# Kernel tuning notes

Hardware: AMD Instinct MI355X
Metric: run time of the kernel (lower is better)

Reference implementation:

```python
import jax, jax.numpy as jnp
import numpy as np

H = 32        # query heads
KVH = 8       # kv heads
HD = 64       # head_dim
N_REP = H // KVH
THETA = 10000.0


def _rope_cos_sin(seq_len, dim):
    # freqs_cis[t, i] = exp(1j * t * theta^{-2i/dim}) -> return cos, sin [S, dim//2]
    inv_freq = 1.0 / (THETA ** (jnp.arange(0, dim, 2, dtype=jnp.float32) / dim))
    t = jnp.arange(seq_len, dtype=jnp.float32)
    freqs = jnp.outer(t, inv_freq)  # [S, dim//2]
    return jnp.cos(freqs), jnp.sin(freqs)


def _apply_rope(x, cos, sin):
    # x: [B, S, h, HD]; pairs are interleaved (even=real, odd=imag)
    xr = x[..., 0::2]
    xi = x[..., 1::2]
    c = cos[None, :, None, :]
    s = sin[None, :, None, :]
    out_r = xr * c - xi * s
    out_i = xr * s + xi * c
    return jnp.stack([out_r, out_i], axis=-1).reshape(x.shape)


def setup_inputs() -> dict:
    key = jax.random.key(0)
    ks = jax.random.split(key, 5)
    D = 2048
    B, S = 1, 2048
    scale = 0.02
    return {
        "hidden_states": jax.random.normal(ks[0], (B, S, D), jnp.float32),
        "Wq": jax.random.normal(ks[1], (D, H * HD), jnp.float32) * scale,
        "Wk": jax.random.normal(ks[2], (D, KVH * HD), jnp.float32) * scale,
        "Wv": jax.random.normal(ks[3], (D, KVH * HD), jnp.float32) * scale,
        "Wo": jax.random.normal(ks[4], (H * HD, D), jnp.float32) * scale,
    }


def reference(hidden_states, Wq, Wk, Wv, Wo):
    B, S, D = hidden_states.shape
    xq = (hidden_states @ Wq).reshape(B, S, H, HD)
    xk = (hidden_states @ Wk).reshape(B, S, KVH, HD)
    xv = (hidden_states @ Wv).reshape(B, S, KVH, HD)

    cos, sin = _rope_cos_sin(S, HD)
    xq = _apply_rope(xq, cos, sin)
    xk = _apply_rope(xk, cos, sin)

    # GQA: expand kv heads (kv head g -> query heads g*N_REP .. g*N_REP+N_REP-1)
    keys = jnp.repeat(xk, N_REP, axis=2)    # [B, S, H, HD]
    values = jnp.repeat(xv, N_REP, axis=2)

    q = xq.transpose(0, 2, 1, 3)      # [B, H, S, HD]
    k = keys.transpose(0, 2, 1, 3)
    v = values.transpose(0, 2, 1, 3)

    scores = jnp.einsum('bhqd,bhkd->bhqk', q, k) / jnp.sqrt(jnp.float32(HD))
    causal = jnp.tril(jnp.ones((S, S), dtype=bool))
    scores = jnp.where(causal[None, None], scores, jnp.float32(-jnp.inf))
    probs = jax.nn.softmax(scores.astype(jnp.float32), axis=-1).astype(q.dtype)

    out = jnp.einsum('bhqk,bhkd->bhqd', probs, v)   # [B, H, S, HD]
    out = out.transpose(0, 2, 1, 3).reshape(B, S, H * HD)
    return out @ Wo
```

## Files before the change

kernel.cpp:

```cpp
#include <hip/hip_runtime.h>


#define S_LEN  2048
#define NH     32
#define NKV    8

typedef __attribute__((ext_vector_type(8))) __bf16 bf16x8;
typedef __attribute__((ext_vector_type(4))) __bf16 bf16x4;
typedef __attribute__((ext_vector_type(4))) float  f32x4;

#define SCALE_LOG2 0.18033688011112042f
#define L2_10K_32  0.41524101186098665f

__device__ __forceinline__ void glds16(const __bf16* g, __bf16* l) {
  __builtin_amdgcn_global_load_lds(
      (const __attribute__((address_space(1))) unsigned int*)g,
      (__attribute__((address_space(3))) unsigned int*)l, 16, 0, 0);
}

__global__ void k_f32_to_bf16(const float* __restrict__ src,
                              __bf16* __restrict__ dst, int n) {
  int i = (blockIdx.x * blockDim.x + threadIdx.x) * 4;
  if (i >= n) return;
  float4 v = *(const float4*)(src + i);
  bf16x4 o;
  o[0] = (__bf16)v.x; o[1] = (__bf16)v.y; o[2] = (__bf16)v.z; o[3] = (__bf16)v.w;
  *(bf16x4*)(dst + i) = o;
}

__global__ void k_wtrans(const float* __restrict__ W, int ldW,
                         __bf16* __restrict__ Wt) {
  __shared__ float t[32][33];
  int n0 = blockIdx.x * 32, k0 = blockIdx.y * 32;
  int tx = threadIdx.x, ty = threadIdx.y;
#pragma unroll
  for (int j = 0; j < 4; j++)
    t[ty + j * 8][tx] = W[(size_t)(k0 + ty + j * 8) * ldW + n0 + tx];
  __syncthreads();
#pragma unroll
  for (int j = 0; j < 4; j++)
    Wt[(size_t)(n0 + ty + j * 8) * 2048 + k0 + tx] = (__bf16)t[tx][ty + j * 8];
}

__global__ void k_vtrans_b(const __bf16* __restrict__ V, __bf16* __restrict__ Vt) {
  __shared__ __bf16 t[32][33];
  int c0 = blockIdx.x * 32, s0 = blockIdx.y * 32;
  int tx = threadIdx.x, ty = threadIdx.y;
#pragma unroll
  for (int j = 0; j < 4; j++)
    t[ty + j * 8][tx] = V[(size_t)(s0 + ty + j * 8) * 512 + c0 + tx];
  __syncthreads();
#pragma unroll
  for (int j = 0; j < 4; j++)
    Vt[(size_t)(c0 + ty + j * 8) * 2048 + s0 + tx] = t[tx][ty + j * 8];
}

__global__ void k_add2(const float* __restrict__ a, const float* __restrict__ b,
                       float* __restrict__ out, int n) {
  int i = (blockIdx.x * blockDim.x + threadIdx.x) * 4;
  if (i >= n) return;
  float4 x = *(const float4*)(a + i);
  float4 y = *(const float4*)(b + i);
  x.x += y.x; x.y += y.y; x.z += y.z; x.w += y.w;
  *(float4*)(out + i) = x;
}

__global__ __launch_bounds__(256) void k_gemm_qkv(
    const __bf16* __restrict__ A, const __bf16* __restrict__ Bt,
    __bf16* __restrict__ Qb, __bf16* __restrict__ Kb, __bf16* __restrict__ Vb) {
  const int K = 2048, N = 3072;
  __shared__ __bf16 As[128][32];
  __shared__ __bf16 Bs[128][32];
  const int tid = threadIdx.x;
  const int m0 = blockIdx.x * 128, n0 = blockIdx.y * 128;
  const int w = tid >> 6, lane = tid & 63, quad = lane >> 4, lid = lane & 15;
  const int wm = (w & 1) * 64, wn = (w >> 1) * 64;
  const int r0 = tid >> 2;
  const int cg = (((tid & 3) ^ ((tid >> 3) & 3)) * 8);
  const __bf16* Ag = A + (size_t)(m0 + r0) * K + cg;
  const __bf16* Bg = Bt + (size_t)(n0 + r0) * K + cg;
  __bf16* Asl = &As[0][0] + tid * 8;
  __bf16* Bsl = &Bs[0][0] + tid * 8;
  const int csw = ((quad ^ ((lid >> 1) & 3)) * 8);
  f32x4 acc[4][4] = {};
  for (int k0 = 0; k0 < K; k0 += 32) {
    __syncthreads();
    glds16(Ag + k0, Asl);
    glds16(Ag + (size_t)64 * K + k0, Asl + 2048);
    glds16(Bg + k0, Bsl);
    glds16(Bg + (size_t)64 * K + k0, Bsl + 2048);
    __syncthreads();
    bf16x8 a[4], b[4];
#pragma unroll
    for (int mt = 0; mt < 4; mt++)
      a[mt] = *(const bf16x8*)(&As[wm + mt * 16 + lid][csw]);
#pragma unroll
    for (int nt = 0; nt < 4; nt++)
      b[nt] = *(const bf16x8*)(&Bs[wn + nt * 16 + lid][csw]);
#pragma unroll
    for (int mt = 0; mt < 4; mt++)
#pragma unroll
      for (int nt = 0; nt < 4; nt++)
        acc[mt][nt] = __builtin_amdgcn_mfma_f32_16x16x32_bf16(
            a[mt], b[nt], acc[mt][nt], 0, 0, 0);
  }
  if (n0 >= 2560) {
#pragma unroll
    for (int mt = 0; mt < 4; mt++)
#pragma unroll
      for (int nt = 0; nt < 4; nt++)
#pragma unroll
        for (int i = 0; i < 4; i++) {
          int mm = m0 + wm + mt * 16 + quad * 4 + i;
          int nn = n0 + wn + nt * 16 + lid - 2560;
          Vb[(size_t)mm * 512 + nn] = (__bf16)acc[mt][nt][i];
        }
  } else {
    const bool isQ = (n0 < 2048);
    const float scale = isQ ? SCALE_LOG2 : 1.0f;
    __bf16* dst = isQ ? Qb : Kb;
    const int ldd = isQ ? 2048 : 512;
    const int noff = isQ ? 0 : 2048;
    const bool odd = lid & 1;
#pragma unroll
    for (int nt = 0; nt < 4; nt++) {
      int nn = n0 + wn + nt * 16 + lid;
      int fi = (nn & 63) >> 1;
      float inv = __builtin_amdgcn_exp2f(-(float)fi * L2_10K_32);
#pragma unroll
      for (int mt = 0; mt < 4; mt++)
#pragma unroll
        for (int i = 0; i < 4; i++) {
          int mm = m0 + wm + mt * 16 + quad * 4 + i;
          float ang = (float)mm * inv;
          float sn, cs;
          __sincosf(ang, &sn, &cs);
          float v = acc[mt][nt][i];
          float p = __shfl_xor(v, 1);
          float o = v * cs + (odd ? p : -p) * sn;
          dst[(size_t)mm * ldd + nn - noff] = (__bf16)(o * scale);
        }
    }
  }
}

__global__ __launch_bounds__(256) void k_gemm(
    const __bf16* __restrict__ A, const __bf16* __restrict__ Bt,
    float* __restrict__ C, int M, int N, int K, int klen) {
  __shared__ __bf16 As[128][32];
  __shared__ __bf16 Bs[128][32];
  const int tid = threadIdx.x;
  const int m0 = blockIdx.x * 128, n0 = blockIdx.y * 128;
  const size_t koff = (size_t)blockIdx.z * klen;
  C += (size_t)blockIdx.z * M * N;
  const int w = tid >> 6, lane = tid & 63, quad = lane >> 4, lid = lane & 15;
  const int wm = (w & 1) * 64, wn = (w >> 1) * 64;
  const int r0 = tid >> 2;
  const int cg = (((tid & 3) ^ ((tid >> 3) & 3)) * 8);
  const __bf16* Ag = A + (size_t)(m0 + r0) * K + koff + cg;
  const __bf16* Bg = Bt + (size_t)(n0 + r0) * K + koff + cg;
  __bf16* Asl = &As[0][0] + tid * 8;
  __bf16* Bsl = &Bs[0][0] + tid * 8;
  const int csw = ((quad ^ ((lid >> 1) & 3)) * 8);
  f32x4 acc[4][4] = {};
  for (int k0 = 0; k0 < klen; k0 += 32) {
    __syncthreads();
    glds16(Ag + k0, Asl);
    glds16(Ag + (size_t)64 * K + k0, Asl + 2048);
    glds16(Bg + k0, Bsl);
    glds16(Bg + (size_t)64 * K + k0, Bsl + 2048);
    __syncthreads();
    bf16x8 a[4], b[4];
#pragma unroll
    for (int mt = 0; mt < 4; mt++)
      a[mt] = *(const bf16x8*)(&As[wm + mt * 16 + lid][csw]);
#pragma unroll
    for (int nt = 0; nt < 4; nt++)
      b[nt] = *(const bf16x8*)(&Bs[wn + nt * 16 + lid][csw]);
#pragma unroll
    for (int mt = 0; mt < 4; mt++)
#pragma unroll
      for (int nt = 0; nt < 4; nt++)
        acc[mt][nt] = __builtin_amdgcn_mfma_f32_16x16x32_bf16(
            a[mt], b[nt], acc[mt][nt], 0, 0, 0);
  }
#pragma unroll
  for (int mt = 0; mt < 4; mt++)
#pragma unroll
    for (int nt = 0; nt < 4; nt++)
#pragma unroll
      for (int i = 0; i < 4; i++) {
        int mm = m0 + wm + mt * 16 + quad * 4 + i;
        int nn = n0 + wn + nt * 16 + lid;
        C[(size_t)mm * N + nn] = acc[mt][nt][i];
      }
}

__global__ __launch_bounds__(256) void k_attn(
    const __bf16* __restrict__ Q, const __bf16* __restrict__ Kc,
    const __bf16* __restrict__ Vt, __bf16* __restrict__ Oc) {
  __shared__ __bf16 Qs[64][64];
  __shared__ __bf16 Ks[2][64][64];
  __shared__ __bf16 Vs[2][64][64];
  __shared__ __bf16 Ps[4][16][72];
  const int h = blockIdx.x;
  const int qt = (gridDim.y - 1) - blockIdx.y;
  const int q0 = qt * 64;
  const int kvh = h >> 2;
  const int tid = threadIdx.x;
  const int w = tid >> 6, lane = tid & 63, quad = lane >> 4, lid = lane & 15;
  const int r0 = tid >> 3;
  const int cg0 = (((tid & 7) ^ (r0 & 7)) * 8);

  const __bf16* Qg = Q + (size_t)(q0 + r0) * 2048 + h * 64 + cg0;
  const __bf16* Kg = Kc + kvh * 64 + cg0;
  const __bf16* Vg = Vt + ((size_t)kvh * 64 + r0) * 2048 + cg0;

  glds16(Qg, &Qs[0][0] + tid * 8);
  glds16(Qg + (size_t)32 * 2048, &Qs[0][0] + (tid + 256) * 8);
  glds16(Kg + (size_t)r0 * 512, &Ks[0][0][0] + tid * 8);
  glds16(Kg + (size_t)(r0 + 32) * 512, &Ks[0][0][0] + (tid + 256) * 8);
  glds16(Vg, &Vs[0][0][0] + tid * 8);
  glds16(Vg + (size_t)32 * 2048, &Vs[0][0][0] + (tid + 256) * 8);
  __syncthreads();

  const int clq = (quad ^ (lid & 7)) * 8;
  bf16x8 aq0 = *(const bf16x8*)(&Qs[w * 16 + lid][clq]);
  bf16x8 aq1 = *(const bf16x8*)(&Qs[w * 16 + lid][clq ^ 32]);
  bf16x8 bone;
#pragma unroll
  for (int j = 0; j < 8; j++) bone[j] = (lid == 0) ? (__bf16)1.0f : (__bf16)0.0f;

  f32x4 Oacc[4] = {};
  f32x4 Lacc = {};
  float mi[4];
#pragma unroll
  for (int i = 0; i < 4; i++) mi[i] = -1e30f;

  for (int kt = 0; kt <= qt; kt++) {
    const int cb = kt & 1;
    if (kt < qt) {
      const int nb = cb ^ 1;
      const size_t kv1 = (size_t)(kt + 1) * 64;
      glds16(Kg + (kv1 + r0) * 512, &Ks[nb][0][0] + tid * 8);
      glds16(Kg + (kv1 + r0 + 32) * 512, &Ks[nb][0][0] + (tid + 256) * 8);
      glds16(Vg + kv1, &Vs[nb][0][0] + tid * 8);
      glds16(Vg + (size_t)32 * 2048 + kv1, &Vs[nb][0][0] + (tid + 256) * 8);
    }

    f32x4 Sc[4] = {};
#pragma unroll
    for (int nt = 0; nt < 4; nt++) {
      bf16x8 b0 = *(const bf16x8*)(&Ks[cb][nt * 16 + lid][clq]);
      bf16x8 b1 = *(const bf16x8*)(&Ks[cb][nt * 16 + lid][clq ^ 32]);
      Sc[nt] = __builtin_amdgcn_mfma_f32_16x16x32_bf16(aq0, b0, Sc[nt], 0, 0, 0);
      Sc[nt] = __builtin_amdgcn_mfma_f32_16x16x32_bf16(aq1, b1, Sc[nt], 0, 0, 0);
    }
    if (kt == qt) {
#pragma unroll
      for (int nt = 0; nt < 4; nt++)
#pragma unroll
        for (int i = 0; i < 4; i++) {
          int kvcol = nt * 16 + lid, qrow = w * 16 + quad * 4 + i;
          if (kvcol > qrow) Sc[nt][i] = -1e30f;
        }
    }

    float alpha[4];
#pragma unroll
    for (int i = 0; i < 4; i++) {
      float m = fmaxf(fmaxf(Sc[0][i], Sc[1][i]), fmaxf(Sc[2][i], Sc[3][i]));
#pragma unroll
      for (int off = 1; off < 16; off <<= 1) m = fmaxf(m, __shfl_xor(m, off));
      float mnew = fmaxf(mi[i], m);
      alpha[i] = __builtin_amdgcn_exp2f(mi[i] - mnew);
      mi[i] = mnew;
    }
#pragma unroll
    for (int nt = 0; nt < 4; nt++)
#pragma unroll
      for (int i = 0; i < 4; i++) {
        float p = __builtin_amdgcn_exp2f(Sc[nt][i] - mi[i]);
        Ps[w][quad * 4 + i][nt * 16 + lid] = (__bf16)p;
      }
#pragma unroll
    for (int nt = 0; nt < 4; nt++)
#pragma unroll
      for (int i = 0; i < 4; i++) Oacc[nt][i] *= alpha[i];
#pragma unroll
    for (int i = 0; i < 4; i++) Lacc[i] *= alpha[i];

#pragma unroll
    for (int kc = 0; kc < 2; kc++) {
      bf16x8 ap = *(const bf16x8*)(&Ps[w][lid][kc * 32 + quad * 8]);
      Lacc = __builtin_amdgcn_mfma_f32_16x16x32_bf16(ap, bone, Lacc, 0, 0, 0);
#pragma unroll
      for (int nt = 0; nt < 4; nt++) {
        bf16x8 bv = *(const bf16x8*)(
            &Vs[cb][nt * 16 + lid][(((kc * 4 + quad) ^ (lid & 7)) * 8)]);
        Oacc[nt] = __builtin_amdgcn_mfma_f32_16x16x32_bf16(ap, bv, Oacc[nt], 0, 0, 0);
      }
    }
    __syncthreads();
  }

#pragma unroll
  for (int nt = 0; nt < 4; nt++)
#pragma unroll
    for (int i = 0; i < 4; i++) {
      float li = __shfl(Lacc[i], lane & 48);
      int qrow = q0 + w * 16 + quad * 4 + i;
      int hd = nt * 16 + lid;
      Oc[(size_t)qrow * 2048 + h * 64 + hd] = (__bf16)(Oacc[nt][i] / li);
    }
}

extern "C" void kernel_launch(void* const* d_in, const int* in_sizes, int n_in,
                              void* d_out, int out_size, void* d_ws, size_t ws_size,
                              hipStream_t stream) {
  const float* hx = (const float*)d_in[0];
  const float* Wq = (const float*)d_in[1];
  const float* Wk = (const float*)d_in[2];
  const float* Wv = (const float*)d_in[3];
  const float* Wo = (const float*)d_in[4];
  float* out = (float*)d_out;

  char* ws = (char*)d_ws;
  size_t off = 0;
  auto alloc = [&](size_t bytes) -> void* {
    void* p = ws + off;
    off += (bytes + 255) & ~(size_t)255;
    return p;
  };
  __bf16* Xb    = (__bf16*)alloc((size_t)2048 * 2048 * 2);
  __bf16* Wqkvt = (__bf16*)alloc((size_t)3072 * 2048 * 2);
  __bf16* Wot   = (__bf16*)alloc((size_t)2048 * 2048 * 2);
  __bf16* Qb    = (__bf16*)alloc((size_t)2048 * 2048 * 2);
  __bf16* Kb    = (__bf16*)alloc((size_t)2048 * 512 * 2);
  __bf16* Vb    = (__bf16*)alloc((size_t)2048 * 512 * 2);
  __bf16* Vtg   = (__bf16*)alloc((size_t)512 * 2048 * 2);
  __bf16* AOb   = (__bf16*)alloc((size_t)2048 * 2048 * 2);
  float*  Cf0   = (float*)alloc((size_t)2048 * 2048 * 4);
  float*  Cf1   = (float*)alloc((size_t)2048 * 2048 * 4);

  k_f32_to_bf16<<<4096, 256, 0, stream>>>(hx, Xb, 2048 * 2048);
  k_wtrans<<<dim3(64, 64), dim3(32, 8), 0, stream>>>(Wq, 2048, Wqkvt);
  k_wtrans<<<dim3(16, 64), dim3(32, 8), 0, stream>>>(Wk, 512, Wqkvt + (size_t)2048 * 2048);
  k_wtrans<<<dim3(16, 64), dim3(32, 8), 0, stream>>>(Wv, 512, Wqkvt + (size_t)2560 * 2048);
  k_wtrans<<<dim3(64, 64), dim3(32, 8), 0, stream>>>(Wo, 2048, Wot);
  k_gemm_qkv<<<dim3(16, 24), 256, 0, stream>>>(Xb, Wqkvt, Qb, Kb, Vb);
  k_vtrans_b<<<dim3(16, 64), dim3(32, 8), 0, stream>>>(Vb, Vtg);
  k_attn<<<dim3(NH, S_LEN / 64), 256, 0, stream>>>(Qb, Kb, Vtg, AOb);
  k_gemm<<<dim3(16, 16, 2), 256, 0, stream>>>(AOb, Wot, Cf0, 2048, 2048, 2048, 1024);
  k_add2<<<4096, 256, 0, stream>>>(Cf0, Cf1, out, 2048 * 2048);
}
```

Baseline: 245.2 us.

## Fuse prep kernels, retile GEMMs, drop split-K, widen attention query tile

Folds the input cast and the four weight transposes into a single prep launch. Shrinks the M tile of both GEMMs to 64 so more blocks run, and drops split-K plus the add kernel so the output GEMM writes the result directly. Attention now processes 128 query rows per block with two m-tiles per wave, uses DPP for the row max and pair swaps, and aliases Q with the P buffer in LDS. Together these cut launches and intermediate traffic and raise data reuse, but the larger attention blocks reduce grid size and may lower occupancy.

```diff
diff --git a/kernel.cpp b/kernel.cpp
--- a/kernel.cpp
+++ b/kernel.cpp
@@ -1,12 +1,10 @@
 #include <hip/hip_runtime.h>
 
 
-#define S_LEN  2048
-#define NH     32
-#define NKV    8
+#define NH  32
+#define NKV 8
 
 typedef __attribute__((ext_vector_type(8))) __bf16 bf16x8;
-typedef __attribute__((ext_vector_type(4))) __bf16 bf16x4;
 typedef __attribute__((ext_vector_type(4))) float  f32x4;
 
 #define SCALE_LOG2 0.18033688011112042f
@@ -18,28 +16,58 @@
       (__attribute__((address_space(3))) unsigned int*)l, 16, 0, 0);
 }
 
-__global__ void k_f32_to_bf16(const float* __restrict__ src,
-                              __bf16* __restrict__ dst, int n) {
-  int i = (blockIdx.x * blockDim.x + threadIdx.x) * 4;
-  if (i >= n) return;
-  float4 v = *(const float4*)(src + i);
-  bf16x4 o;
-  o[0] = (__bf16)v.x; o[1] = (__bf16)v.y; o[2] = (__bf16)v.z; o[3] = (__bf16)v.w;
-  *(bf16x4*)(dst + i) = o;
-}
-
-__global__ void k_wtrans(const float* __restrict__ W, int ldW,
-                         __bf16* __restrict__ Wt) {
+__device__ __forceinline__ float qmax16(float v) {
+  int t;
+  t = __builtin_amdgcn_mov_dpp(__builtin_bit_cast(int, v), 0x128, 0xf, 0xf, true);
+  v = fmaxf(v, __builtin_bit_cast(float, t));
+  t = __builtin_amdgcn_mov_dpp(__builtin_bit_cast(int, v), 0x124, 0xf, 0xf, true);
+  v = fmaxf(v, __builtin_bit_cast(float, t));
+  t = __builtin_amdgcn_mov_dpp(__builtin_bit_cast(int, v), 0x122, 0xf, 0xf, true);
+  v = fmaxf(v, __builtin_bit_cast(float, t));
+  t = __builtin_amdgcn_mov_dpp(__builtin_bit_cast(int, v), 0x121, 0xf, 0xf, true);
+  v = fmaxf(v, __builtin_bit_cast(float, t));
+  return v;
+}
+
+__device__ __forceinline__ float pair_swap(float v) {
+  int t = __builtin_amdgcn_mov_dpp(__builtin_bit_cast(int, v), 0xB1, 0xf, 0xf, true);
+  return __builtin_bit_cast(float, t);
+}
+
+__device__ __forceinline__ unsigned pack_bf16(float lo, float hi) {
+  union { __bf16 b[2]; unsigned u; } r;
+  r.b[0] = (__bf16)lo; r.b[1] = (__bf16)hi;
+  return r.u;
+}
+
+__global__ void k_prep(const float* __restrict__ hx, const float* __restrict__ Wq,
+                       const float* __restrict__ Wk, const float* __restrict__ Wv,
+                       const float* __restrict__ Wo, __bf16* __restrict__ Xb,
+                       __bf16* __restrict__ Wqkvt, __bf16* __restrict__ Wot) {
   __shared__ float t[32][33];
-  int n0 = blockIdx.x * 32, k0 = blockIdx.y * 32;
-  int tx = threadIdx.x, ty = threadIdx.y;
+  const int nt = blockIdx.x, k0 = blockIdx.y * 32;
+  const int tx = threadIdx.x, ty = threadIdx.y;
+  if (nt >= 160) {
+    int c0 = (nt - 160) * 32;
+#pragma unroll
+    for (int j = 0; j < 4; j++) {
+      size_t idx = (size_t)(k0 + ty + j * 8) * 2048 + c0 + tx;
+      Xb[idx] = (__bf16)hx[idx];
+    }
+    return;
+  }
+  const float* W; int ldW, n0; __bf16* dst;
+  if (nt < 64)      { W = Wq; ldW = 2048; dst = Wqkvt;                        n0 = nt * 32; }
+  else if (nt < 80) { W = Wk; ldW = 512;  dst = Wqkvt + (size_t)2048 * 2048;  n0 = (nt - 64) * 32; }
+  else if (nt < 96) { W = Wv; ldW = 512;  dst = Wqkvt + (size_t)2560 * 2048;  n0 = (nt - 80) * 32; }
+  else              { W = Wo; ldW = 2048; dst = Wot;                          n0 = (nt - 96) * 32; }
 #pragma unroll
   for (int j = 0; j < 4; j++)
     t[ty + j * 8][tx] = W[(size_t)(k0 + ty + j * 8) * ldW + n0 + tx];
   __syncthreads();
 #pragma unroll
   for (int j = 0; j < 4; j++)
-    Wt[(size_t)(n0 + ty + j * 8) * 2048 + k0 + tx] = (__bf16)t[tx][ty + j * 8];
+    dst[(size_t)(n0 + ty + j * 8) * 2048 + k0 + tx] = (__bf16)t[tx][ty + j * 8];
 }
 
 __global__ void k_vtrans_b(const __bf16* __restrict__ V, __bf16* __restrict__ Vt) {
@@ -55,26 +83,16 @@
     Vt[(size_t)(c0 + ty + j * 8) * 2048 + s0 + tx] = t[tx][ty + j * 8];
 }
 
-__global__ void k_add2(const float* __restrict__ a, const float* __restrict__ b,
-                       float* __restrict__ out, int n) {
-  int i = (blockIdx.x * blockDim.x + threadIdx.x) * 4;
-  if (i >= n) return;
-  float4 x = *(const float4*)(a + i);
-  float4 y = *(const float4*)(b + i);
-  x.x += y.x; x.y += y.y; x.z += y.z; x.w += y.w;
-  *(float4*)(out + i) = x;
-}
-
 __global__ __launch_bounds__(256) void k_gemm_qkv(
     const __bf16* __restrict__ A, const __bf16* __restrict__ Bt,
     __bf16* __restrict__ Qb, __bf16* __restrict__ Kb, __bf16* __restrict__ Vb) {
-  const int K = 2048, N = 3072;
-  __shared__ __bf16 As[128][32];
+  const int K = 2048;
+  __shared__ __bf16 As[64][32];
   __shared__ __bf16 Bs[128][32];
   const int tid = threadIdx.x;
-  const int m0 = blockIdx.x * 128, n0 = blockIdx.y * 128;
+  const int m0 = blockIdx.x * 64, n0 = blockIdx.y * 128;
   const int w = tid >> 6, lane = tid & 63, quad = lane >> 4, lid = lane & 15;
-  const int wm = (w & 1) * 64, wn = (w >> 1) * 64;
+  const int wm = (w & 1) * 32, wn = (w >> 1) * 64;
   const int r0 = tid >> 2;
   const int cg = (((tid & 3) ^ ((tid >> 3) & 3)) * 8);
   const __bf16* Ag = A + (size_t)(m0 + r0) * K + cg;
@@ -82,23 +100,22 @@
   __bf16* Asl = &As[0][0] + tid * 8;
   __bf16* Bsl = &Bs[0][0] + tid * 8;
   const int csw = ((quad ^ ((lid >> 1) & 3)) * 8);
-  f32x4 acc[4][4] = {};
+  f32x4 acc[2][4] = {};
   for (int k0 = 0; k0 < K; k0 += 32) {
     __syncthreads();
     glds16(Ag + k0, Asl);
-    glds16(Ag + (size_t)64 * K + k0, Asl + 2048);
     glds16(Bg + k0, Bsl);
     glds16(Bg + (size_t)64 * K + k0, Bsl + 2048);
     __syncthreads();
-    bf16x8 a[4], b[4];
-#pragma unroll
-    for (int mt = 0; mt < 4; mt++)
+    bf16x8 a[2], b[4];
+#pragma unroll
+    for (int mt = 0; mt < 2; mt++)
       a[mt] = *(const bf16x8*)(&As[wm + mt * 16 + lid][csw]);
 #pragma unroll
     for (int nt = 0; nt < 4; nt++)
       b[nt] = *(const bf16x8*)(&Bs[wn + nt * 16 + lid][csw]);
 #pragma unroll
-    for (int mt = 0; mt < 4; mt++)
+    for (int mt = 0; mt < 2; mt++)
 #pragma unroll
       for (int nt = 0; nt < 4; nt++)
         acc[mt][nt] = __builtin_amdgcn_mfma_f32_16x16x32_bf16(
@@ -106,7 +123,7 @@
   }
   if (n0 >= 2560) {
 #pragma unroll
-    for (int mt = 0; mt < 4; mt++)
+    for (int mt = 0; mt < 2; mt++)
 #pragma unroll
       for (int nt = 0; nt < 4; nt++)
 #pragma unroll
@@ -128,7 +145,7 @@
       int fi = (nn & 63) >> 1;
       float inv = __builtin_amdgcn_exp2f(-(float)fi * L2_10K_32);
 #pragma unroll
-      for (int mt = 0; mt < 4; mt++)
+      for (int mt = 0; mt < 2; mt++)
 #pragma unroll
         for (int i = 0; i < 4; i++) {
           int mm = m0 + wm + mt * 16 + quad * 4 + i;
@@ -144,48 +161,46 @@
   }
 }
 
-__global__ __launch_bounds__(256) void k_gemm(
+__global__ __launch_bounds__(256) void k_gemm_out(
     const __bf16* __restrict__ A, const __bf16* __restrict__ Bt,
-    float* __restrict__ C, int M, int N, int K, int klen) {
-  __shared__ __bf16 As[128][32];
+    float* __restrict__ C) {
+  const int K = 2048, N = 2048;
+  __shared__ __bf16 As[64][32];
   __shared__ __bf16 Bs[128][32];
   const int tid = threadIdx.x;
-  const int m0 = blockIdx.x * 128, n0 = blockIdx.y * 128;
-  const size_t koff = (size_t)blockIdx.z * klen;
-  C += (size_t)blockIdx.z * M * N;
+  const int m0 = blockIdx.x * 64, n0 = blockIdx.y * 128;
   const int w = tid >> 6, lane = tid & 63, quad = lane >> 4, lid = lane & 15;
-  const int wm = (w & 1) * 64, wn = (w >> 1) * 64;
+  const int wm = (w & 1) * 32, wn = (w >> 1) * 64;
   const int r0 = tid >> 2;
   const int cg = (((tid & 3) ^ ((tid >> 3) & 3)) * 8);
-  const __bf16* Ag = A + (size_t)(m0 + r0) * K + koff + cg;
-  const __bf16* Bg = Bt + (size_t)(n0 + r0) * K + koff + cg;
+  const __bf16* Ag = A + (size_t)(m0 + r0) * K + cg;
+  const __bf16* Bg = Bt + (size_t)(n0 + r0) * K + cg;
   __bf16* Asl = &As[0][0] + tid * 8;
   __bf16* Bsl = &Bs[0][0] + tid * 8;
   const int csw = ((quad ^ ((lid >> 1) & 3)) * 8);
-  f32x4 acc[4][4] = {};
-  for (int k0 = 0; k0 < klen; k0 += 32) {
+  f32x4 acc[2][4] = {};
+  for (int k0 = 0; k0 < K; k0 += 32) {
     __syncthreads();
     glds16(Ag + k0, Asl);
-    glds16(Ag + (size_t)64 * K + k0, Asl + 2048);
     glds16(Bg + k0, Bsl);
     glds16(Bg + (size_t)64 * K + k0, Bsl + 2048);
     __syncthreads();
-    bf16x8 a[4], b[4];
-#pragma unroll
-    for (int mt = 0; mt < 4; mt++)
+    bf16x8 a[2], b[4];
+#pragma unroll
+    for (int mt = 0; mt < 2; mt++)
       a[mt] = *(const bf16x8*)(&As[wm + mt * 16 + lid][csw]);
 #pragma unroll
     for (int nt = 0; nt < 4; nt++)
       b[nt] = *(const bf16x8*)(&Bs[wn + nt * 16 + lid][csw]);
 #pragma unroll
-    for (int mt = 0; mt < 4; mt++)
+    for (int mt = 0; mt < 2; mt++)
 #pragma unroll
       for (int nt = 0; nt < 4; nt++)
         acc[mt][nt] = __builtin_amdgcn_mfma_f32_16x16x32_bf16(
             a[mt], b[nt], acc[mt][nt], 0, 0, 0);
   }
 #pragma unroll
-  for (int mt = 0; mt < 4; mt++)
+  for (int mt = 0; mt < 2; mt++)
 #pragma unroll
     for (int nt = 0; nt < 4; nt++)
 #pragma unroll
@@ -199,13 +214,15 @@
 __global__ __launch_bounds__(256) void k_attn(
     const __bf16* __restrict__ Q, const __bf16* __restrict__ Kc,
     const __bf16* __restrict__ Vt, __bf16* __restrict__ Oc) {
-  __shared__ __bf16 Qs[64][64];
-  __shared__ __bf16 Ks[2][64][64];
-  __shared__ __bf16 Vs[2][64][64];
-  __shared__ __bf16 Ps[4][16][72];
+  __shared__ char smem[51200];
+  __bf16* PsB = (__bf16*)smem;
+  __bf16* QsB = (__bf16*)smem;
+  __bf16* KsB = (__bf16*)(smem + 18432);
+  __bf16* VsB = (__bf16*)(smem + 34816);
   const int h = blockIdx.x;
-  const int qt = (gridDim.y - 1) - blockIdx.y;
-  const int q0 = qt * 64;
+  const int qt = 15 - blockIdx.y;
+  const int q0 = qt * 128;
+  const int nkv = 2 * qt + 2;
   const int kvh = h >> 2;
   const int tid = threadIdx.x;
   const int w = tid >> 6, lane = tid & 63, quad = lane >> 4, lid = lane & 15;
@@ -214,104 +231,158 @@
 
   const __bf16* Qg = Q + (size_t)(q0 + r0) * 2048 + h * 64 + cg0;
   const __bf16* Kg = Kc + kvh * 64 + cg0;
-  const __bf16* Vg = Vt + ((size_t)kvh * 64 + r0) * 2048 + cg0;
-
-  glds16(Qg, &Qs[0][0] + tid * 8);
-  glds16(Qg + (size_t)32 * 2048, &Qs[0][0] + (tid + 256) * 8);
-  glds16(Kg + (size_t)r0 * 512, &Ks[0][0][0] + tid * 8);
-  glds16(Kg + (size_t)(r0 + 32) * 512, &Ks[0][0][0] + (tid + 256) * 8);
-  glds16(Vg, &Vs[0][0][0] + tid * 8);
-  glds16(Vg + (size_t)32 * 2048, &Vs[0][0][0] + (tid + 256) * 8);
+  const __bf16* Vg = Vt + ((size_t)(kvh * 64 + r0)) * 2048 + cg0;
+
+  glds16(Qg,                     QsB + tid * 8);
+  glds16(Qg + (size_t)32 * 2048, QsB + (tid + 256) * 8);
+  glds16(Qg + (size_t)64 * 2048, QsB + (tid + 512) * 8);
+  glds16(Qg + (size_t)96 * 2048, QsB + (tid + 768) * 8);
+  glds16(Kg + (size_t)r0 * 512,        KsB + tid * 8);
+  glds16(Kg + (size_t)(r0 + 32) * 512, KsB + (tid + 256) * 8);
+  glds16(Vg,                     VsB + tid * 8);
+  glds16(Vg + (size_t)32 * 2048, VsB + (tid + 256) * 8);
   __syncthreads();
 
-  const int clq = (quad ^ (lid & 7)) * 8;
-  bf16x8 aq0 = *(const bf16x8*)(&Qs[w * 16 + lid][clq]);
-  bf16x8 aq1 = *(const bf16x8*)(&Qs[w * 16 + lid][clq ^ 32]);
+  bf16x8 aq[2][2];
+#pragma unroll
+  for (int mt = 0; mt < 2; mt++) {
+    int row = w * 32 + mt * 16 + lid;
+    int cl = (quad ^ (row & 7)) * 8;
+    aq[mt][0] = *(const bf16x8*)(QsB + row * 64 + cl);
+    aq[mt][1] = *(const bf16x8*)(QsB + row * 64 + (cl ^ 32));
+  }
+  __syncthreads();
+
   bf16x8 bone;
 #pragma unroll
   for (int j = 0; j < 8; j++) bone[j] = (lid == 0) ? (__bf16)1.0f : (__bf16)0.0f;
 
-  f32x4 Oacc[4] = {};
-  f32x4 Lacc = {};
-  float mi[4];
-#pragma unroll
-  for (int i = 0; i < 4; i++) mi[i] = -1e30f;
-
-  for (int kt = 0; kt <= qt; kt++) {
+  f32x4 Oacc[2][4] = {};
+  f32x4 Lacc[2] = {};
+  float mi[2][4];
+#pragma unroll
+  for (int mt = 0; mt < 2; mt++)
+#pragma unroll
+    for (int i = 0; i < 4; i++) mi[mt][i] = -1e30f;
+
+  for (int kt = 0; kt < nkv; kt++) {
     const int cb = kt & 1;
-    if (kt < qt) {
+    if (kt + 1 < nkv) {
       const int nb = cb ^ 1;
       const size_t kv1 = (size_t)(kt + 1) * 64;
-      glds16(Kg + (kv1 + r0) * 512, &Ks[nb][0][0] + tid * 8);
-      glds16(Kg + (kv1 + r0 + 32) * 512, &Ks[nb][0][0] + (tid + 256) * 8);
-      glds16(Vg + kv1, &Vs[nb][0][0] + tid * 8);
-      glds16(Vg + (size_t)32 * 2048 + kv1, &Vs[nb][0][0] + (tid + 256) * 8);
-    }
-
-    f32x4 Sc[4] = {};
+      glds16(Kg + (kv1 + r0) * 512,        KsB + nb * 4096 + tid * 8);
+      glds16(Kg + (kv1 + r0 + 32) * 512,   KsB + nb * 4096 + (tid + 256) * 8);
+      glds16(Vg + kv1,                     VsB + nb * 4096 + tid * 8);
+      glds16(Vg + (size_t)32 * 2048 + kv1, VsB + nb * 4096 + (tid + 256) * 8);
+    }
+
+    f32x4 Sc[2][4] = {};
 #pragma unroll
     for (int nt = 0; nt < 4; nt++) {
-      bf16x8 b0 = *(const bf16x8*)(&Ks[cb][nt * 16 + lid][clq]);
-      bf16x8 b1 = *(const bf16x8*)(&Ks[cb][nt * 16 + lid][clq ^ 32]);
-      Sc[nt] = __builtin_amdgcn_mfma_f32_16x16x32_bf16(aq0, b0, Sc[nt], 0, 0, 0);
-      Sc[nt] = __builtin_amdgcn_mfma_f32_16x16x32_bf16(aq1, b1, Sc[nt], 0, 0, 0);
-    }
-    if (kt == qt) {
+      int row = nt * 16 + lid;
+      int cl = (quad ^ (lid & 7)) * 8;
+      bf16x8 b0 = *(const bf16x8*)(KsB + cb * 4096 + row * 64 + cl);
+      bf16x8 b1 = *(const bf16x8*)(KsB + cb * 4096 + row * 64 + (cl ^ 32));
+#pragma unroll
+      for (int mt = 0; mt < 2; mt++) {
+        Sc[mt][nt] = __builtin_amdgcn_mfma_f32_16x16x32_bf16(aq[mt][0], b0, Sc[mt][nt], 0, 0, 0);
+        Sc[mt][nt] = __builtin_amdgcn_mfma_f32_16x16x32_bf16(aq[mt][1], b1, Sc[mt][nt], 0, 0, 0);
+      }
+    }
+    if (kt >= nkv - 2) {
+#pragma unroll
+      for (int mt = 0; mt < 2; mt++)
+#pragma unroll
+        for (int nt = 0; nt < 4; nt++)
+#pragma unroll
+          for (int i = 0; i < 4; i++) {
+            int kvg = kt * 64 + nt * 16 + lid;
+            int qrg = q0 + w * 32 + mt * 16 + quad * 4 + i;
+            if (kvg > qrg) Sc[mt][nt][i] = -1e30f;
+          }
+    }
+
+    float alpha[2][4];
+#pragma unroll
+    for (int mt = 0; mt < 2; mt++)
+#pragma unroll
+      for (int i = 0; i < 4; i++) {
+        float m = fmaxf(fmaxf(Sc[mt][0][i], Sc[mt][1][i]),
+                        fmaxf(Sc[mt][2][i], Sc[mt][3][i]));
+        m = qmax16(m);
+        float mnew = fmaxf(mi[mt][i], m);
+        alpha[mt][i] = __builtin_amdgcn_exp2f(mi[mt][i] - mnew);
+        mi[mt][i] = mnew;
+      }
+#pragma unroll
+    for (int mt = 0; mt < 2; mt++)
 #pragma unroll
       for (int nt = 0; nt < 4; nt++)
 #pragma unroll
+        for (int i = 0; i < 4; i++)
+          Sc[mt][nt][i] = __builtin_amdgcn_exp2f(Sc[mt][nt][i] - mi[mt][i]);
+
+#pragma unroll
+    for (int mt = 0; mt < 2; mt++)
+#pragma unroll
+      for (int t = 0; t < 2; t++)
+#pragma unroll
         for (int i = 0; i < 4; i++) {
-          int kvcol = nt * 16 + lid, qrow = w * 16 + quad * 4 + i;
-          if (kvcol > qrow) Sc[nt][i] = -1e30f;
+          float pA = Sc[mt][2 * t][i], pB = Sc[mt][2 * t + 1][i];
+          float send = (lid & 1) ? pA : pB;
+          float recv = pair_swap(send);
+          float lo = (lid & 1) ? recv : pA;
+          float hi = (lid & 1) ? pB : recv;
+          int row = mt * 16 + quad * 4 + i;
+          int col = t * 32 + ((lid & 1) ? (lid + 15) : lid);
+          *(unsigned*)(PsB + (size_t)w * 2304 + row * 72 + col) = pack_bf16(lo, hi);
         }
-    }
-
-    float alpha[4];
+
+#pragma unroll
+    for (int mt = 0; mt < 2; mt++) {
+#pragma unroll
+      for (int nt = 0; nt < 4; nt++)
+#pragma unroll
+        for (int i = 0; i < 4; i++) Oacc[mt][nt][i] *= alpha[mt][i];
+#pragma unroll
+      for (int i = 0; i < 4; i++) Lacc[mt][i] *= alpha[mt][i];
+    }
+
+#pragma unroll
+    for (int kc = 0; kc < 2; kc++) {
+      bf16x8 ap[2];
+#pragma unroll
+      for (int mt = 0; mt < 2; mt++)
+        ap[mt] = *(const bf16x8*)(PsB + (size_t)w * 2304 + (mt * 16 + lid) * 72 +
+                                  kc * 32 + quad * 8);
+#pragma unroll
+      for (int mt = 0; mt < 2; mt++)
+        Lacc[mt] = __builtin_amdgcn_mfma_f32_16x16x32_bf16(ap[mt], bone, Lacc[mt], 0, 0, 0);
+#pragma unroll
+      for (int nt = 0; nt < 4; nt++) {
+        int row = nt * 16 + lid;
+        int cl = (((kc * 4 + quad) ^ (lid & 7)) * 8);
+        bf16x8 bv = *(const bf16x8*)(VsB + cb * 4096 + row * 64 + cl);
+#pragma unroll
+        for (int mt = 0; mt < 2; mt++)
+          Oacc[mt][nt] = __builtin_amdgcn_mfma_f32_16x16x32_bf16(ap[mt], bv, Oacc[mt][nt], 0, 0, 0);
+      }
+    }
+    __syncthreads();
+  }
+
+#pragma unroll
+  for (int mt = 0; mt < 2; mt++)
 #pragma unroll
     for (int i = 0; i < 4; i++) {
-      float m = fmaxf(fmaxf(Sc[0][i], Sc[1][i]), fmaxf(Sc[2][i], Sc[3][i]));
-#pragma unroll
-      for (int off = 1; off < 16; off <<= 1) m = fmaxf(m, __shfl_xor(m, off));
-      float mnew = fmaxf(mi[i], m);
-      alpha[i] = __builtin_amdgcn_exp2f(mi[i] - mnew);
-      mi[i] = mnew;
-    }
-#pragma unroll
-    for (int nt = 0; nt < 4; nt++)
-#pragma unroll
-      for (int i = 0; i < 4; i++) {
-        float p = __builtin_amdgcn_exp2f(Sc[nt][i] - mi[i]);
-        Ps[w][quad * 4 + i][nt * 16 + lid] = (__bf16)p;
+      float li = __shfl(Lacc[mt][i], lane & 48);
+      float r = 1.0f / li;
+#pragma unroll
+      for (int nt = 0; nt < 4; nt++) {
+        int qrow = q0 + w * 32 + mt * 16 + quad * 4 + i;
+        int hd = nt * 16 + lid;
+        Oc[(size_t)qrow * 2048 + h * 64 + hd] = (__bf16)(Oacc[mt][nt][i] * r);
       }
-#pragma unroll
-    for (int nt = 0; nt < 4; nt++)
-#pragma unroll
-      for (int i = 0; i < 4; i++) Oacc[nt][i] *= alpha[i];
-#pragma unroll
-    for (int i = 0; i < 4; i++) Lacc[i] *= alpha[i];
-
-#pragma unroll
-    for (int kc = 0; kc < 2; kc++) {
-      bf16x8 ap = *(const bf16x8*)(&Ps[w][lid][kc * 32 + quad * 8]);
-      Lacc = __builtin_amdgcn_mfma_f32_16x16x32_bf16(ap, bone, Lacc, 0, 0, 0);
-#pragma unroll
-      for (int nt = 0; nt < 4; nt++) {
-        bf16x8 bv = *(const bf16x8*)(
-            &Vs[cb][nt * 16 + lid][(((kc * 4 + quad) ^ (lid & 7)) * 8)]);
-        Oacc[nt] = __builtin_amdgcn_mfma_f32_16x16x32_bf16(ap, bv, Oacc[nt], 0, 0, 0);
-      }
-    }
-    __syncthreads();
-  }
-
-#pragma unroll
-  for (int nt = 0; nt < 4; nt++)
-#pragma unroll
-    for (int i = 0; i < 4; i++) {
-      float li = __shfl(Lacc[i], lane & 48);
-      int qrow = q0 + w * 16 + quad * 4 + i;
-      int hd = nt * 16 + lid;
-      Oc[(size_t)qrow * 2048 + h * 64 + hd] = (__bf16)(Oacc[nt][i] / li);
     }
 }
 
@@ -340,17 +411,11 @@
   __bf16* Vb    = (__bf16*)alloc((size_t)2048 * 512 * 2);
   __bf16* Vtg   = (__bf16*)alloc((size_t)512 * 2048 * 2);
   __bf16* AOb   = (__bf16*)alloc((size_t)2048 * 2048 * 2);
-  float*  Cf0   = (float*)alloc((size_t)2048 * 2048 * 4);
-  float*  Cf1   = (float*)alloc((size_t)2048 * 2048 * 4);
-
-  k_f32_to_bf16<<<4096, 256, 0, stream>>>(hx, Xb, 2048 * 2048);
-  k_wtrans<<<dim3(64, 64), dim3(32, 8), 0, stream>>>(Wq, 2048, Wqkvt);
-  k_wtrans<<<dim3(16, 64), dim3(32, 8), 0, stream>>>(Wk, 512, Wqkvt + (size_t)2048 * 2048);
-  k_wtrans<<<dim3(16, 64), dim3(32, 8), 0, stream>>>(Wv, 512, Wqkvt + (size_t)2560 * 2048);
-  k_wtrans<<<dim3(64, 64), dim3(32, 8), 0, stream>>>(Wo, 2048, Wot);
-  k_gemm_qkv<<<dim3(16, 24), 256, 0, stream>>>(Xb, Wqkvt, Qb, Kb, Vb);
+
+  k_prep<<<dim3(224, 64), dim3(32, 8), 0, stream>>>(hx, Wq, Wk, Wv, Wo,
+                                                    Xb, Wqkvt, Wot);
+  k_gemm_qkv<<<dim3(32, 24), 256, 0, stream>>>(Xb, Wqkvt, Qb, Kb, Vb);
   k_vtrans_b<<<dim3(16, 64), dim3(32, 8), 0, stream>>>(Vb, Vtg);
-  k_attn<<<dim3(NH, S_LEN / 64), 256, 0, stream>>>(Qb, Kb, Vtg, AOb);
-  k_gemm<<<dim3(16, 16, 2), 256, 0, stream>>>(AOb, Wot, Cf0, 2048, 2048, 2048, 1024);
-  k_add2<<<4096, 256, 0, stream>>>(Cf0, Cf1, out, 2048 * 2048);
-}
+  k_attn<<<dim3(NH, 16), 256, 0, stream>>>(Qb, Kb, Vtg, AOb);
+  k_gemm_out<<<dim3(32, 16), 256, 0, stream>>>(AOb, Wot, out);
+}
```

New measurement: 238.5 us. -2.7%, faster.
